# Performance work log

Hardware: AMD Instinct MI355X
Metric: run time of the kernel (lower is better)

Reference implementation:

```python
import jax, jax.numpy as jnp
import numpy as np


def setup_inputs() -> dict:
    key = jax.random.key(0)
    k1, k2, k3 = jax.random.split(key, 3)
    B, H, D, N = 2, 16, 64, 2048
    return {
        "query": jax.random.normal(k1, (B, H, D, N), dtype=jnp.float32),
        "key": jax.random.normal(k2, (B, H, D, N), dtype=jnp.float32),
        "value": jax.random.normal(k3, (B, H, D, N), dtype=jnp.float32),
    }


def reference(query, key, value):
    # NOTE: original torch code scales by sqrt(query.size(-1)) which,
    # given the [B,H,d,N] layout, is sqrt(N) (the sequence length), not sqrt(d).
    scale = query.shape[-1] ** 0.5
    # scores[b,h,q,k] = sum_d query[b,h,d,q] * key[b,h,d,k]
    scores = jnp.einsum("bhdq,bhdk->bhqk", query, key) / scale
    attn = jax.nn.softmax(scores, axis=-1)
    # out[b,h,q,v] = sum_k attn[b,h,q,k] * value[b,h,v,k]
    return jnp.einsum("bhqk,bhvk->bhqv", attn, value)
```

## Files before the change

kernel.cpp:

```cpp
#include <hip/hip_runtime.h>
#include <hip/hip_bf16.h>


typedef __attribute__((ext_vector_type(8))) short short8;
typedef __attribute__((ext_vector_type(4))) float f32x4;

#define NN 2048
#define DD 64

#if __has_builtin(__builtin_amdgcn_exp2f)
#define EXP2(x) __builtin_amdgcn_exp2f(x)
#else
#define EXP2(x) __expf(0.69314718056f * (x))
#endif

__device__ __forceinline__ unsigned pk2(float a, float b) {
  __hip_bfloat162 h = __float22bfloat162_rn(make_float2(a, b));
  unsigned u; __builtin_memcpy(&u, &h, 4); return u;
}
__device__ __forceinline__ short f2bf(float f) {
  union { float f; unsigned u; } x; x.f = f;
  unsigned r = (x.u + 0x7fffu + ((x.u >> 16) & 1u)) >> 16;
  return (short)r;
}

__global__ __launch_bounds__(256, 2) void attn_kernel(
    const float* __restrict__ Q, const float* __restrict__ K,
    const float* __restrict__ V, float* __restrict__ Out) {
  const int tid  = threadIdx.x;
  const int wave = tid >> 6, lane = tid & 63;
  const int quad = lane >> 4, l16 = lane & 15;
  const int sw   = l16 & 7;

  const int xcd  = blockIdx.x & 7, slot = blockIdx.x >> 3;
  const int bh   = xcd * 4 + (slot >> 4);
  const int qblk = slot & 15;

  const float* Qh = Q + (size_t)bh * DD * NN;
  const float* Kh = K + (size_t)bh * DD * NN;
  const float* Vh = V + (size_t)bh * DD * NN;
  float*       Oh = Out + (size_t)bh * NN * DD;

  __shared__ __align__(16) char ldsK[2][64 * 128];
  __shared__ __align__(16) char ldsV[2][64 * 128];
  __shared__ __align__(16) char ldsP[8][16 * 128];

  const float qscale = 0.031881407f;
  short8 bQ[2][2];
  int qb[2];
#pragma unroll
  for (int qt = 0; qt < 2; ++qt) {
    qb[qt] = qblk * 128 + (wave * 2 + qt) * 16;
#pragma unroll
    for (int h = 0; h < 2; ++h)
#pragma unroll
      for (int j = 0; j < 8; ++j) {
        int d = h * 32 + quad * 8 + j;
        bQ[qt][h][j] = f2bf(Qh[(size_t)d * NN + qb[qt] + l16] * qscale);
      }
  }

  f32x4 accO[2][4];
#pragma unroll
  for (int qt = 0; qt < 2; ++qt)
#pragma unroll
    for (int vt = 0; vt < 4; ++vt) accO[qt][vt] = (f32x4){0.f, 0.f, 0.f, 0.f};
  float lp[2] = {0.f, 0.f};

  const int da  = tid & 15;
  const int kb4 = (tid >> 4) * 4;
  const int vv  = tid >> 2;
  const int vko = (tid & 3) * 16;
  const float* kbase = Kh + (size_t)(da * 4) * NN + kb4;
  const float* vbase = Vh + (size_t)vv * NN + vko;
  char* Pq0 = ldsP[wave * 2];
  char* Pq1 = ldsP[wave * 2 + 1];

  float kreg[4][4];
  float4 vf0, vf1, vf2, vf3;
  auto load_kv = [&](int k0) {
#pragma unroll
    for (int i = 0; i < 4; ++i) {
      float4 t = *(const float4*)(kbase + (size_t)i * NN + k0);
      kreg[i][0] = t.x; kreg[i][1] = t.y; kreg[i][2] = t.z; kreg[i][3] = t.w;
    }
    const float4* pv = (const float4*)(vbase + k0);
    vf0 = pv[0]; vf1 = pv[1]; vf2 = pv[2]; vf3 = pv[3];
  };
  auto store_kv = [&](char* bK, char* bV) {
#pragma unroll
    for (int j = 0; j < 4; ++j) {
      int key = kb4 + j;
      int phys = (da >> 1) ^ (key & 7);
      uint2 w; w.x = pk2(kreg[0][j], kreg[1][j]); w.y = pk2(kreg[2][j], kreg[3][j]);
      *(uint2*)&bK[key * 128 + phys * 16 + (da & 1) * 8] = w;
    }
    int ph0 = ((vko >> 3))     ^ (vv & 7);
    int ph1 = ((vko >> 3) + 1) ^ (vv & 7);
    uint4 w0 = make_uint4(pk2(vf0.x, vf0.y), pk2(vf0.z, vf0.w),
                          pk2(vf1.x, vf1.y), pk2(vf1.z, vf1.w));
    uint4 w1 = make_uint4(pk2(vf2.x, vf2.y), pk2(vf2.z, vf2.w),
                          pk2(vf3.x, vf3.y), pk2(vf3.z, vf3.w));
    *(uint4*)&bV[vv * 128 + ph0 * 16] = w0;
    *(uint4*)&bV[vv * 128 + ph1 * 16] = w1;
  };

  load_kv(0);
  store_kv(ldsK[0], ldsV[0]);
  __syncthreads();

  for (int it = 0; it < 32; ++it) {
    const int cur = it & 1;
    load_kv(((it + 1) & 31) * 64);

    const char* cK = ldsK[cur];
    const char* cV = ldsV[cur];

    f32x4 s[2][4];
#pragma unroll
    for (int kt = 0; kt < 4; ++kt) {
      const int key = kt * 16 + l16;
      short8 aK0 = *(const short8*)&cK[key * 128 + ((quad)     ^ sw) * 16];
      short8 aK1 = *(const short8*)&cK[key * 128 + ((quad + 4) ^ sw) * 16];
      f32x4 z = (f32x4){0.f, 0.f, 0.f, 0.f};
      s[0][kt] = __builtin_amdgcn_mfma_f32_16x16x32_bf16(aK0, bQ[0][0], z, 0, 0, 0);
      s[0][kt] = __builtin_amdgcn_mfma_f32_16x16x32_bf16(aK1, bQ[0][1], s[0][kt], 0, 0, 0);
      s[1][kt] = __builtin_amdgcn_mfma_f32_16x16x32_bf16(aK0, bQ[1][0], z, 0, 0, 0);
      s[1][kt] = __builtin_amdgcn_mfma_f32_16x16x32_bf16(aK1, bQ[1][1], s[1][kt], 0, 0, 0);
    }

#pragma unroll
    for (int qt = 0; qt < 2; ++qt) {
      char* Pq = qt ? Pq1 : Pq0;
#pragma unroll
      for (int kt = 0; kt < 4; ++kt) {
        float p0 = EXP2(s[qt][kt][0]);
        float p1 = EXP2(s[qt][kt][1]);
        float p2 = EXP2(s[qt][kt][2]);
        float p3 = EXP2(s[qt][kt][3]);
        lp[qt] += (p0 + p1) + (p2 + p3);
        uint2 w; w.x = pk2(p0, p1); w.y = pk2(p2, p3);
        int phys = ((kt << 1) | (quad >> 1)) ^ sw;
        *(uint2*)&Pq[l16 * 128 + phys * 16 + (quad & 1) * 8] = w;
      }
    }

#pragma unroll
    for (int h2 = 0; h2 < 2; ++h2) {
      const int pg = (h2 * 4 + quad) ^ sw;
      short8 aP0 = *(const short8*)&Pq0[l16 * 128 + pg * 16];
      short8 aP1 = *(const short8*)&Pq1[l16 * 128 + pg * 16];
#pragma unroll
      for (int vt = 0; vt < 4; ++vt) {
        short8 bV = *(const short8*)&cV[(vt * 16 + l16) * 128 + pg * 16];
        accO[0][vt] = __builtin_amdgcn_mfma_f32_16x16x32_bf16(aP0, bV, accO[0][vt], 0, 0, 0);
        accO[1][vt] = __builtin_amdgcn_mfma_f32_16x16x32_bf16(aP1, bV, accO[1][vt], 0, 0, 0);
      }
    }

    store_kv(ldsK[cur ^ 1], ldsV[cur ^ 1]);
    __syncthreads();
  }

#pragma unroll
  for (int qt = 0; qt < 2; ++qt) {
    float l = lp[qt];
    l += __shfl_xor(l, 16, 64);
    l += __shfl_xor(l, 32, 64);
#pragma unroll
    for (int r = 0; r < 4; ++r) {
      float lr  = __shfl(l, quad * 4 + r, 64);
      float inv = 1.0f / lr;
      int q = qb[qt] + quad * 4 + r;
#pragma unroll
      for (int vt = 0; vt < 4; ++vt)
        Oh[(size_t)q * DD + vt * 16 + l16] = accO[qt][vt][r] * inv;
    }
  }
}

extern "C" void kernel_launch(void* const* d_in, const int* in_sizes, int n_in,
                              void* d_out, int out_size, void* d_ws, size_t ws_size,
                              hipStream_t stream) {
  const float* Q = (const float*)d_in[0];
  const float* K = (const float*)d_in[1];
  const float* V = (const float*)d_in[2];
  float* O = (float*)d_out;
  dim3 grid(2 * 16 * (NN / 128));
  attn_kernel<<<grid, dim3(256), 0, stream>>>(Q, K, V, O);
}
```

Before: 141.9 us.

## Split key range across two blocks with atomic accumulation and separate normalization

Each block now handles half of the keys for its query tile, which doubles the grid to 1024 blocks. Partial outputs and row sums are accumulated with global atomicAdd into zeroed buffers, and a separate norm kernel divides by the sums afterwards. The P tile in LDS is halved to one per wave, V fragments are hoisted into registers, and launch bounds allow four blocks per CU. In exchange the change adds two memsets, atomic traffic, an extra kernel launch and a read-modify-write pass over the output.

```diff
diff --git a/kernel.cpp b/kernel.cpp
--- a/kernel.cpp
+++ b/kernel.cpp
@@ -24,26 +24,30 @@
   return (short)r;
 }
 
-__global__ __launch_bounds__(256, 2) void attn_kernel(
+__global__ __launch_bounds__(256, 4) void attn_kernel(
     const float* __restrict__ Q, const float* __restrict__ K,
-    const float* __restrict__ V, float* __restrict__ Out) {
+    const float* __restrict__ V, float* __restrict__ Oacc,
+    float* __restrict__ lws) {
   const int tid  = threadIdx.x;
   const int wave = tid >> 6, lane = tid & 63;
   const int quad = lane >> 4, l16 = lane & 15;
   const int sw   = l16 & 7;
 
   const int xcd  = blockIdx.x & 7, slot = blockIdx.x >> 3;
-  const int bh   = xcd * 4 + (slot >> 4);
-  const int qblk = slot & 15;
+  const int bh   = xcd * 4 + (slot >> 5);
+  const int rem  = slot & 31;
+  const int qblk = rem >> 1;
+  const int kh   = rem & 1;
+  const int kbeg = kh * (NN / 2);
 
   const float* Qh = Q + (size_t)bh * DD * NN;
   const float* Kh = K + (size_t)bh * DD * NN;
   const float* Vh = V + (size_t)bh * DD * NN;
-  float*       Oh = Out + (size_t)bh * NN * DD;
+  float*       Oh = Oacc + (size_t)bh * NN * DD;
 
   __shared__ __align__(16) char ldsK[2][64 * 128];
   __shared__ __align__(16) char ldsV[2][64 * 128];
-  __shared__ __align__(16) char ldsP[8][16 * 128];
+  __shared__ __align__(16) char ldsP[4][16 * 128];
 
   const float qscale = 0.031881407f;
   short8 bQ[2][2];
@@ -71,10 +75,9 @@
   const int kb4 = (tid >> 4) * 4;
   const int vv  = tid >> 2;
   const int vko = (tid & 3) * 16;
-  const float* kbase = Kh + (size_t)(da * 4) * NN + kb4;
-  const float* vbase = Vh + (size_t)vv * NN + vko;
-  char* Pq0 = ldsP[wave * 2];
-  char* Pq1 = ldsP[wave * 2 + 1];
+  const float* kbase = Kh + (size_t)(da * 4) * NN + kbeg + kb4;
+  const float* vbase = Vh + (size_t)vv * NN + kbeg + vko;
+  char* Pq = ldsP[wave];
 
   float kreg[4][4];
   float4 vf0, vf1, vf2, vf3;
@@ -109,9 +112,9 @@
   store_kv(ldsK[0], ldsV[0]);
   __syncthreads();
 
-  for (int it = 0; it < 32; ++it) {
+  for (int it = 0; it < 16; ++it) {
     const int cur = it & 1;
-    load_kv(((it + 1) & 31) * 64);
+    load_kv(((it + 1) & 15) * 64);
 
     const char* cK = ldsK[cur];
     const char* cV = ldsV[cur];
@@ -129,9 +132,17 @@
       s[1][kt] = __builtin_amdgcn_mfma_f32_16x16x32_bf16(aK1, bQ[1][1], s[1][kt], 0, 0, 0);
     }
 
+    short8 bV[2][4];
+#pragma unroll
+    for (int h2 = 0; h2 < 2; ++h2) {
+      const int pg = (h2 * 4 + quad) ^ sw;
+#pragma unroll
+      for (int vt = 0; vt < 4; ++vt)
+        bV[h2][vt] = *(const short8*)&cV[(vt * 16 + l16) * 128 + pg * 16];
+    }
+
 #pragma unroll
     for (int qt = 0; qt < 2; ++qt) {
-      char* Pq = qt ? Pq1 : Pq0;
 #pragma unroll
       for (int kt = 0; kt < 4; ++kt) {
         float p0 = EXP2(s[qt][kt][0]);
@@ -143,18 +154,14 @@
         int phys = ((kt << 1) | (quad >> 1)) ^ sw;
         *(uint2*)&Pq[l16 * 128 + phys * 16 + (quad & 1) * 8] = w;
       }
-    }
-
-#pragma unroll
-    for (int h2 = 0; h2 < 2; ++h2) {
-      const int pg = (h2 * 4 + quad) ^ sw;
-      short8 aP0 = *(const short8*)&Pq0[l16 * 128 + pg * 16];
-      short8 aP1 = *(const short8*)&Pq1[l16 * 128 + pg * 16];
-#pragma unroll
-      for (int vt = 0; vt < 4; ++vt) {
-        short8 bV = *(const short8*)&cV[(vt * 16 + l16) * 128 + pg * 16];
-        accO[0][vt] = __builtin_amdgcn_mfma_f32_16x16x32_bf16(aP0, bV, accO[0][vt], 0, 0, 0);
-        accO[1][vt] = __builtin_amdgcn_mfma_f32_16x16x32_bf16(aP1, bV, accO[1][vt], 0, 0, 0);
+#pragma unroll
+      for (int h2 = 0; h2 < 2; ++h2) {
+        const int pg = (h2 * 4 + quad) ^ sw;
+        short8 aP = *(const short8*)&Pq[l16 * 128 + pg * 16];
+#pragma unroll
+        for (int vt = 0; vt < 4; ++vt)
+          accO[qt][vt] = __builtin_amdgcn_mfma_f32_16x16x32_bf16(aP, bV[h2][vt],
+                                                                accO[qt][vt], 0, 0, 0);
       }
     }
 
@@ -167,16 +174,25 @@
     float l = lp[qt];
     l += __shfl_xor(l, 16, 64);
     l += __shfl_xor(l, 32, 64);
+    if (quad == 0)
+      atomicAdd(&lws[(size_t)bh * NN + qb[qt] + l16], l);
 #pragma unroll
     for (int r = 0; r < 4; ++r) {
-      float lr  = __shfl(l, quad * 4 + r, 64);
-      float inv = 1.0f / lr;
       int q = qb[qt] + quad * 4 + r;
 #pragma unroll
       for (int vt = 0; vt < 4; ++vt)
-        Oh[(size_t)q * DD + vt * 16 + l16] = accO[qt][vt][r] * inv;
+        atomicAdd(&Oh[(size_t)q * DD + vt * 16 + l16], accO[qt][vt][r]);
     }
   }
+}
+
+__global__ __launch_bounds__(256) void norm_kernel(float* __restrict__ out,
+                                                   const float* __restrict__ lws) {
+  int i = blockIdx.x * 256 + threadIdx.x;
+  float4 v = ((const float4*)out)[i];
+  float inv = 1.0f / lws[i >> 4];
+  v.x *= inv; v.y *= inv; v.z *= inv; v.w *= inv;
+  ((float4*)out)[i] = v;
 }
 
 extern "C" void kernel_launch(void* const* d_in, const int* in_sizes, int n_in,
@@ -185,7 +201,10 @@
   const float* Q = (const float*)d_in[0];
   const float* K = (const float*)d_in[1];
   const float* V = (const float*)d_in[2];
-  float* O = (float*)d_out;
-  dim3 grid(2 * 16 * (NN / 128));
-  attn_kernel<<<grid, dim3(256), 0, stream>>>(Q, K, V, O);
-}
+  float* O   = (float*)d_out;
+  float* lws = (float*)d_ws;
+  hipMemsetAsync(d_out, 0, (size_t)out_size * sizeof(float), stream);
+  hipMemsetAsync(d_ws, 0, (size_t)2 * 16 * NN * sizeof(float), stream);
+  attn_kernel<<<dim3(1024), dim3(256), 0, stream>>>(Q, K, V, O, lws);
+  norm_kernel<<<dim3(out_size / 4 / 256), dim3(256), 0, stream>>>(O, lws);
+}
```

Result: slower. 165.3 us (+16.5%).

## Keep softmax probabilities in registers by permuting V layout in LDS

Applied to the files above, without the earlier changes.

Drops the LDS round trip for the P tile. The probability fragment from the QK MFMA is packed straight into registers as the A operand of the PV MFMA. To keep that valid, the V staging layout in LDS is permuted so each 8-key group the MFMA reads matches the key order each lane holds in registers. This removes LDS writes and reads for P and frees shared memory, in exchange for narrower 8-byte V stores and a more intricate layout coupling that must stay correct.

```diff
diff --git a/kernel.cpp b/kernel.cpp
--- a/kernel.cpp
+++ b/kernel.cpp
@@ -43,7 +43,6 @@
 
   __shared__ __align__(16) char ldsK[2][64 * 128];
   __shared__ __align__(16) char ldsV[2][64 * 128];
-  __shared__ __align__(16) char ldsP[8][16 * 128];
 
   const float qscale = 0.031881407f;
   short8 bQ[2][2];
@@ -71,10 +70,10 @@
   const int kb4 = (tid >> 4) * 4;
   const int vv  = tid >> 2;
   const int vko = (tid & 3) * 16;
+  const int vg32 = vko >> 5;
+  const int vh   = (vko >> 4) & 1;
   const float* kbase = Kh + (size_t)(da * 4) * NN + kb4;
   const float* vbase = Vh + (size_t)vv * NN + vko;
-  char* Pq0 = ldsP[wave * 2];
-  char* Pq1 = ldsP[wave * 2 + 1];
 
   float kreg[4][4];
   float4 vf0, vf1, vf2, vf3;
@@ -95,14 +94,18 @@
       uint2 w; w.x = pk2(kreg[0][j], kreg[1][j]); w.y = pk2(kreg[2][j], kreg[3][j]);
       *(uint2*)&bK[key * 128 + phys * 16 + (da & 1) * 8] = w;
     }
-    int ph0 = ((vko >> 3))     ^ (vv & 7);
-    int ph1 = ((vko >> 3) + 1) ^ (vv & 7);
-    uint4 w0 = make_uint4(pk2(vf0.x, vf0.y), pk2(vf0.z, vf0.w),
-                          pk2(vf1.x, vf1.y), pk2(vf1.z, vf1.w));
-    uint4 w1 = make_uint4(pk2(vf2.x, vf2.y), pk2(vf2.z, vf2.w),
-                          pk2(vf3.x, vf3.y), pk2(vf3.z, vf3.w));
-    *(uint4*)&bV[vv * 128 + ph0 * 16] = w0;
-    *(uint4*)&bV[vv * 128 + ph1 * 16] = w1;
+    {
+      uint2 w0, w1, w2, w3;
+      w0.x = pk2(vf0.x, vf0.y); w0.y = pk2(vf0.z, vf0.w);
+      w1.x = pk2(vf1.x, vf1.y); w1.y = pk2(vf1.z, vf1.w);
+      w2.x = pk2(vf2.x, vf2.y); w2.y = pk2(vf2.z, vf2.w);
+      w3.x = pk2(vf3.x, vf3.y); w3.y = pk2(vf3.z, vf3.w);
+      char* row = bV + vv * 128 + vh * 8;
+      *(uint2*)&row[(((vg32 << 2) | 0) ^ (vv & 7)) * 16] = w0;
+      *(uint2*)&row[(((vg32 << 2) | 1) ^ (vv & 7)) * 16] = w1;
+      *(uint2*)&row[(((vg32 << 2) | 2) ^ (vv & 7)) * 16] = w2;
+      *(uint2*)&row[(((vg32 << 2) | 3) ^ (vv & 7)) * 16] = w3;
+    }
   };
 
   load_kv(0);
@@ -129,32 +132,37 @@
       s[1][kt] = __builtin_amdgcn_mfma_f32_16x16x32_bf16(aK1, bQ[1][1], s[1][kt], 0, 0, 0);
     }
 
+    short8 aP[2][2];
 #pragma unroll
     for (int qt = 0; qt < 2; ++qt) {
-      char* Pq = qt ? Pq1 : Pq0;
+      float p[4][4];
 #pragma unroll
       for (int kt = 0; kt < 4; ++kt) {
-        float p0 = EXP2(s[qt][kt][0]);
-        float p1 = EXP2(s[qt][kt][1]);
-        float p2 = EXP2(s[qt][kt][2]);
-        float p3 = EXP2(s[qt][kt][3]);
-        lp[qt] += (p0 + p1) + (p2 + p3);
-        uint2 w; w.x = pk2(p0, p1); w.y = pk2(p2, p3);
-        int phys = ((kt << 1) | (quad >> 1)) ^ sw;
-        *(uint2*)&Pq[l16 * 128 + phys * 16 + (quad & 1) * 8] = w;
+        p[kt][0] = EXP2(s[qt][kt][0]);
+        p[kt][1] = EXP2(s[qt][kt][1]);
+        p[kt][2] = EXP2(s[qt][kt][2]);
+        p[kt][3] = EXP2(s[qt][kt][3]);
+        lp[qt] += (p[kt][0] + p[kt][1]) + (p[kt][2] + p[kt][3]);
+      }
+#pragma unroll
+      for (int h2 = 0; h2 < 2; ++h2) {
+        uint4 u;
+        u.x = pk2(p[2 * h2][0],     p[2 * h2][1]);
+        u.y = pk2(p[2 * h2][2],     p[2 * h2][3]);
+        u.z = pk2(p[2 * h2 + 1][0], p[2 * h2 + 1][1]);
+        u.w = pk2(p[2 * h2 + 1][2], p[2 * h2 + 1][3]);
+        __builtin_memcpy(&aP[qt][h2], &u, 16);
       }
     }
 
 #pragma unroll
     for (int h2 = 0; h2 < 2; ++h2) {
       const int pg = (h2 * 4 + quad) ^ sw;
-      short8 aP0 = *(const short8*)&Pq0[l16 * 128 + pg * 16];
-      short8 aP1 = *(const short8*)&Pq1[l16 * 128 + pg * 16];
 #pragma unroll
       for (int vt = 0; vt < 4; ++vt) {
         short8 bV = *(const short8*)&cV[(vt * 16 + l16) * 128 + pg * 16];
-        accO[0][vt] = __builtin_amdgcn_mfma_f32_16x16x32_bf16(aP0, bV, accO[0][vt], 0, 0, 0);
-        accO[1][vt] = __builtin_amdgcn_mfma_f32_16x16x32_bf16(aP1, bV, accO[1][vt], 0, 0, 0);
+        accO[0][vt] = __builtin_amdgcn_mfma_f32_16x16x32_bf16(aP[0][h2], bV, accO[0][vt], 0, 0, 0);
+        accO[1][vt] = __builtin_amdgcn_mfma_f32_16x16x32_bf16(aP[1][h2], bV, accO[1][vt], 0, 0, 0);
       }
     }
 
```

Measured after the change: 169.8 us. +19.7%, slower.
